# Performance work log

Hardware: AMD Instinct MI355X
Metric: run time of the kernel (lower is better)

## Reference

```python
import jax, jax.numpy as jnp
import numpy as np

N_USERS = 100000
N_ITEMS = 100000
NNZ = 3200000
D = 128

def _spmm(rows, cols, vals, dense, n_out):
    # COO SpMM: out[r] += vals * dense[c]
    gathered = dense[cols] * vals[:, None]  # [nnz, D]
    return jax.ops.segment_sum(gathered, rows, num_segments=n_out)

def setup_inputs() -> dict:
    key = jax.random.key(0)
    ks = jax.random.split(key, 7)
    return {
        "input": jax.random.normal(ks[0], (N_USERS + N_ITEMS, D), dtype=jnp.float32),
        "user_rows": jax.random.randint(ks[1], (NNZ,), 0, N_USERS, dtype=jnp.int32),
        "user_cols": jax.random.randint(ks[2], (NNZ,), 0, N_USERS, dtype=jnp.int32),
        "user_vals": jax.random.uniform(ks[3], (NNZ,), dtype=jnp.float32),
        "item_rows": jax.random.randint(ks[4], (NNZ,), 0, N_ITEMS, dtype=jnp.int32),
        "item_cols": jax.random.randint(ks[5], (NNZ,), 0, N_ITEMS, dtype=jnp.int32),
        "item_vals": jax.random.uniform(ks[6], (NNZ,), dtype=jnp.float32),
    }

def reference(input, user_rows, user_cols, user_vals, item_rows, item_cols, item_vals):
    users_emb = input[:N_USERS]          # [n_users, D]
    items_emb = input[N_USERS:]          # [n_items, D]
    h_u1 = _spmm(user_rows, user_cols, user_vals, users_emb, N_USERS)
    h_i1 = _spmm(item_rows, item_cols, item_vals, items_emb, N_ITEMS)
    return jnp.concatenate([h_u1, h_i1], axis=0)
```

## Files before the change

### kernel.cpp

```cpp
#include <hip/hip_runtime.h>

#define NU   100000
#define NI   100000
#define NNZE 3200000
#define D    128
#define CAPB 80

__device__ __forceinline__ unsigned bf15(float v) {
    return ((__float_as_uint(v) + 0x8000u) >> 16) & 0x7FFFu;
}
__device__ __forceinline__ unsigned bf16r(float x) {
    unsigned u = __float_as_uint(x);
    return (u + 0x7FFFu + ((u >> 16) & 1u)) >> 16;
}

__global__ void cvt_kernel(const float* __restrict__ in, unsigned short* __restrict__ outb) {
    const int total = (NU + NI) * D / 8;
    int gid = blockIdx.x * blockDim.x + threadIdx.x;
    const int stride = gridDim.x * blockDim.x;
    for (int i = gid; i < total; i += stride) {
        const float4 a = reinterpret_cast<const float4*>(in)[2 * i];
        const float4 b = reinterpret_cast<const float4*>(in)[2 * i + 1];
        uint4 w;
        w.x = bf16r(a.x) | (bf16r(a.y) << 16);
        w.y = bf16r(a.z) | (bf16r(a.w) << 16);
        w.z = bf16r(b.x) | (bf16r(b.y) << 16);
        w.w = bf16r(b.z) | (bf16r(b.w) << 16);
        reinterpret_cast<uint4*>(outb)[i] = w;
    }
}

__global__ void build_bins_kernel(const int* __restrict__ urows,
                                  const int* __restrict__ ucols,
                                  const float* __restrict__ uvals,
                                  const int* __restrict__ irows,
                                  const int* __restrict__ icols,
                                  const float* __restrict__ ivals,
                                  int* __restrict__ cnt_u, int* __restrict__ cnt_i,
                                  unsigned* __restrict__ bin_u, unsigned* __restrict__ bin_i,
                                  int cap) {
    int gid = blockIdx.x * blockDim.x + threadIdx.x;
    int stride = gridDim.x * blockDim.x;
    for (int e = gid; e < NNZE; e += stride) {
        int r = urows[e];
        int p = atomicAdd(&cnt_u[r], 1);
        if (p < cap) bin_u[(size_t)r * cap + p] = ((unsigned)ucols[e] << 15) | bf15(uvals[e]);
        r = irows[e];
        p = atomicAdd(&cnt_i[r], 1);
        if (p < cap) bin_i[(size_t)r * cap + p] = ((unsigned)icols[e] << 15) | bf15(ivals[e]);
    }
}

__global__ void pull_bf16_kernel(const unsigned short* __restrict__ tabb,
                                 const int* __restrict__ cnt_u, const int* __restrict__ cnt_i,
                                 const unsigned* __restrict__ bin_u,
                                 const unsigned* __restrict__ bin_i,
                                 float* __restrict__ out, int cap) {
    const int wid = (int)(((size_t)blockIdx.x * blockDim.x + threadIdx.x) >> 6);
    if (wid >= NU + NI) return;
    const int lane = threadIdx.x & 63;
    const int q    = lane >> 4;
    const int s16  = lane & 15;
    const int* cnt; const unsigned* bin; const unsigned short* src; float* dst; int row;
    if (wid < NU) {
        cnt = cnt_u; bin = bin_u; src = tabb; dst = out; row = wid;
    } else {
        cnt = cnt_i; bin = bin_i;
        src = tabb + (size_t)NU * D; dst = out + (size_t)NU * D; row = wid - NU;
    }
    int n = cnt[row];
    if (n > cap) n = cap;
    const unsigned* brow = bin + (size_t)row * cap;
    float acc[8];
#pragma unroll
    for (int k = 0; k < 8; ++k) acc[k] = 0.f;

    for (int base = 0; base < n; base += 64) {
        int m = n - base; if (m > 64) m = 64;
        unsigned ent = 0;
        if (lane < m) ent = brow[base + lane];
        const int   c = (int)(ent >> 15);
        const float v = __uint_as_float((ent & 0x7FFFu) << 16);

        int j = 0;
        for (; j + 8 <= m; j += 8) {
            const int   c0 = __shfl(c, j + q),     c1 = __shfl(c, j + 4 + q);
            const float v0 = __shfl(v, j + q),     v1 = __shfl(v, j + 4 + q);
            const uint4 x0 = reinterpret_cast<const uint4*>(src + (size_t)c0 * D)[s16];
            const uint4 x1 = reinterpret_cast<const uint4*>(src + (size_t)c1 * D)[s16];
#pragma unroll
            for (int t = 0; t < 4; ++t) {
                const unsigned u0 = (&x0.x)[t], u1 = (&x1.x)[t];
                acc[2*t]   += __uint_as_float(u0 << 16)         * v0;
                acc[2*t+1] += __uint_as_float(u0 & 0xFFFF0000u) * v0;
                acc[2*t]   += __uint_as_float(u1 << 16)         * v1;
                acc[2*t+1] += __uint_as_float(u1 & 0xFFFF0000u) * v1;
            }
        }
        for (; j + 4 <= m; j += 4) {
            const int   cc = __shfl(c, j + q);
            const float vv = __shfl(v, j + q);
            const uint4 x = reinterpret_cast<const uint4*>(src + (size_t)cc * D)[s16];
#pragma unroll
            for (int t = 0; t < 4; ++t) {
                const unsigned u = (&x.x)[t];
                acc[2*t]   += __uint_as_float(u << 16)         * vv;
                acc[2*t+1] += __uint_as_float(u & 0xFFFF0000u) * vv;
            }
        }
        if (j < m) {
            const int jj = j + q;
            const int   cc = __shfl(c, (jj < m) ? jj : j);
            const float vv = __shfl(v, (jj < m) ? jj : j);
            if (jj < m) {
                const uint4 x = reinterpret_cast<const uint4*>(src + (size_t)cc * D)[s16];
#pragma unroll
                for (int t = 0; t < 4; ++t) {
                    const unsigned u = (&x.x)[t];
                    acc[2*t]   += __uint_as_float(u << 16)         * vv;
                    acc[2*t+1] += __uint_as_float(u & 0xFFFF0000u) * vv;
                }
            }
        }
    }
#pragma unroll
    for (int k = 0; k < 8; ++k) {
        acc[k] += __shfl_xor(acc[k], 16);
        acc[k] += __shfl_xor(acc[k], 32);
    }
    if (q == 0) {
        float4 o0, o1;
        o0.x = acc[0]; o0.y = acc[1]; o0.z = acc[2]; o0.w = acc[3];
        o1.x = acc[4]; o1.y = acc[5]; o1.z = acc[6]; o1.w = acc[7];
        float4* op = reinterpret_cast<float4*>(dst + (size_t)row * D + 8 * s16);
        op[0] = o0; op[1] = o1;
    }
}

__global__ void hist_kernel(const int* __restrict__ urows,
                            const int* __restrict__ irows,
                            int* __restrict__ cnt_u, int* __restrict__ cnt_i) {
    int gid = blockIdx.x * blockDim.x + threadIdx.x;
    int stride = gridDim.x * blockDim.x;
    for (int e = gid; e < NNZE; e += stride) {
        atomicAdd(&cnt_u[urows[e]], 1);
        atomicAdd(&cnt_i[irows[e]], 1);
    }
}

__global__ void scan_kernel(int* __restrict__ cnt_u, int* __restrict__ off_u,
                            int* __restrict__ cnt_i, int* __restrict__ off_i) {
    int* cnt = (blockIdx.x == 0) ? cnt_u : cnt_i;
    int* off = (blockIdx.x == 0) ? off_u : off_i;
    const int n = (blockIdx.x == 0) ? NU : NI;
    __shared__ int lds[1024];
    int carry = 0;
    for (int base = 0; base < n; base += 1024) {
        const int i = base + (int)threadIdx.x;
        const int v = (i < n) ? cnt[i] : 0;
        lds[threadIdx.x] = v;
        __syncthreads();
        for (int ofs = 1; ofs < 1024; ofs <<= 1) {
            int t = (threadIdx.x >= (unsigned)ofs) ? lds[threadIdx.x - ofs] : 0;
            __syncthreads();
            lds[threadIdx.x] += t;
            __syncthreads();
        }
        const int incl = lds[threadIdx.x];
        const int excl = incl - v;
        if (i < n) {
            off[i] = carry + excl;
            cnt[i] = carry + excl;
        }
        carry += lds[1023];
        __syncthreads();
    }
    if (threadIdx.x == 0) off[n] = carry;
}

__global__ void scatter_kernel(const int* __restrict__ urows,
                               const int* __restrict__ irows,
                               int* __restrict__ cur_u, int* __restrict__ cur_i,
                               int* __restrict__ perm_u, int* __restrict__ perm_i) {
    int gid = blockIdx.x * blockDim.x + threadIdx.x;
    int stride = gridDim.x * blockDim.x;
    for (int e = gid; e < NNZE; e += stride) {
        int p = atomicAdd(&cur_u[urows[e]], 1);
        perm_u[p] = e;
        p = atomicAdd(&cur_i[irows[e]], 1);
        perm_i[p] = e;
    }
}

__global__ void pull_csr_kernel(const float* __restrict__ input,
                                const int* __restrict__ ucols, const float* __restrict__ uvals,
                                const int* __restrict__ icols, const float* __restrict__ ivals,
                                const int* __restrict__ off_u, const int* __restrict__ perm_u,
                                const int* __restrict__ off_i, const int* __restrict__ perm_i,
                                float* __restrict__ out) {
    const int wid = (int)(((size_t)blockIdx.x * blockDim.x + threadIdx.x) >> 6);
    if (wid >= NU + NI) return;
    const int lane = threadIdx.x & 63;
    const int* off; const int* perm; const int* cols; const float* vals;
    const float* src; float* dst; int row;
    if (wid < NU) {
        off = off_u; perm = perm_u; cols = ucols; vals = uvals;
        src = input; dst = out; row = wid;
    } else {
        off = off_i; perm = perm_i; cols = icols; vals = ivals;
        src = input + (size_t)NU * D; dst = out + (size_t)NU * D; row = wid - NU;
    }
    const int s = off[row];
    const int n = off[row + 1] - s;
    float accx = 0.f, accy = 0.f;
    for (int base = 0; base < n; base += 64) {
        int m = n - base; if (m > 64) m = 64;
        int c = 0; float v = 0.f;
        if (lane < m) {
            const int nz = perm[s + base + lane];
            c = cols[nz];
            v = vals[nz];
        }
        for (int j = 0; j < m; ++j) {
            const int   cc = __shfl(c, j);
            const float vv = __shfl(v, j);
            const float2 x = reinterpret_cast<const float2*>(src + (size_t)cc * D)[lane];
            accx += x.x * vv; accy += x.y * vv;
        }
    }
    float2 o; o.x = accx; o.y = accy;
    reinterpret_cast<float2*>(dst + (size_t)row * D)[lane] = o;
}

__global__ void spmm_scatter_kernel(const float* __restrict__ input,
                                    const int* __restrict__ urows,
                                    const int* __restrict__ ucols,
                                    const float* __restrict__ uvals,
                                    const int* __restrict__ irows,
                                    const int* __restrict__ icols,
                                    const float* __restrict__ ivals,
                                    float* __restrict__ out) {
    const long long total = 2LL * NNZE * 32;
    long long gid = (long long)blockIdx.x * blockDim.x + threadIdx.x;
    const long long stride = (long long)gridDim.x * blockDim.x;
    for (; gid < total; gid += stride) {
        const int e = (int)(gid >> 5);
        const int qq = (int)(gid & 31);
        int row, col; float val; const float* src; float* dst;
        if (e < NNZE) {
            row = urows[e]; col = ucols[e]; val = uvals[e];
            src = input; dst = out;
        } else {
            const int e2 = e - NNZE;
            row = irows[e2]; col = icols[e2]; val = ivals[e2];
            src = input + (long long)NU * D; dst = out + (long long)NU * D;
        }
        const float4 v = reinterpret_cast<const float4*>(src + (long long)col * D)[qq];
        float* o = dst + (long long)row * D + (qq << 2);
        atomicAdd(o + 0, v.x * val);
        atomicAdd(o + 1, v.y * val);
        atomicAdd(o + 2, v.z * val);
        atomicAdd(o + 3, v.w * val);
    }
}

extern "C" void kernel_launch(void* const* d_in, const int* in_sizes, int n_in,
                              void* d_out, int out_size, void* d_ws, size_t ws_size,
                              hipStream_t stream) {
    const float* input = (const float*)d_in[0];
    const int*   urows = (const int*)d_in[1];
    const int*   ucols = (const int*)d_in[2];
    const float* uvals = (const float*)d_in[3];
    const int*   irows = (const int*)d_in[4];
    const int*   icols = (const int*)d_in[5];
    const float* ivals = (const float*)d_in[6];
    float*       out   = (float*)d_out;

    const size_t need_t1 = (size_t)(NU + NI) * 4
                         + (size_t)(NU + NI) * D * 2
                         + (size_t)(NU + NI) * CAPB * 4;
    const size_t need_csr = ((size_t)NU + NI + (NU + 1) + (NI + 1) + 2 * (size_t)NNZE) * 4;

    if (ws_size >= need_t1) {
        int* cnt_u = (int*)d_ws;
        int* cnt_i = cnt_u + NU;
        unsigned short* tabb = (unsigned short*)(cnt_i + NI);
        unsigned* bin_u = (unsigned*)(tabb + (size_t)(NU + NI) * D);
        unsigned* bin_i = bin_u + (size_t)NU * CAPB;

        hipMemsetAsync(cnt_u, 0, (size_t)(NU + NI) * sizeof(int), stream);
        build_bins_kernel<<<4096, 256, 0, stream>>>(
            urows, ucols, uvals, irows, icols, ivals, cnt_u, cnt_i, bin_u, bin_i, CAPB);
        cvt_kernel<<<4096, 256, 0, stream>>>(input, tabb);
        const int blocks = (NU + NI + 3) / 4;
        pull_bf16_kernel<<<blocks, 256, 0, stream>>>(
            tabb, cnt_u, cnt_i, bin_u, bin_i, out, CAPB);
    } else if (ws_size >= need_csr) {
        int* cur_u  = (int*)d_ws;
        int* cur_i  = cur_u + NU;
        int* off_u  = cur_i + NI;
        int* off_i  = off_u + (NU + 1);
        int* perm_u = off_i + (NI + 1);
        int* perm_i = perm_u + NNZE;

        hipMemsetAsync(cur_u, 0, (size_t)(NU + NI) * sizeof(int), stream);
        hist_kernel<<<2048, 256, 0, stream>>>(urows, irows, cur_u, cur_i);
        scan_kernel<<<2, 1024, 0, stream>>>(cur_u, off_u, cur_i, off_i);
        scatter_kernel<<<2048, 256, 0, stream>>>(urows, irows, cur_u, cur_i, perm_u, perm_i);
        const int blocks = (NU + NI + 3) / 4;
        pull_csr_kernel<<<blocks, 256, 0, stream>>>(
            input, ucols, uvals, icols, ivals, off_u, perm_u, off_i, perm_i, out);
    } else {
        hipMemsetAsync(out, 0, (size_t)out_size * sizeof(float), stream);
        spmm_scatter_kernel<<<8192, 256, 0, stream>>>(
            input, urows, ucols, uvals, irows, icols, ivals, out);
    }
}
```

Baseline: 561.9 us.

## Partition bin-building atomics by row residue to localize them per XCD

The bin-build kernel now assigns each block a group g = blockIdx&7, and each block only handles edges whose row satisfies row&7==g. The counter array is re-indexed so each group's counters are contiguous. Since blocks are dispatched round-robin across the 8 XCDs, this aims to keep each counter's atomics and bin writes inside one XCD's L2, cutting cross-die coherence traffic. In exchange, every block reads all edge rows, so row-index reads rise eightfold, and col/val loads become divergent.

New measurement: 603.1 us. 1.07x slower.

```diff
diff --git a/kernel.cpp b/kernel.cpp
--- a/kernel.cpp
+++ b/kernel.cpp
@@ -5,6 +5,7 @@
 #define NNZE 3200000
 #define D    128
 #define CAPB 80
+#define GDIV 12500
 
 __device__ __forceinline__ unsigned bf15(float v) {
     return ((__float_as_uint(v) + 0x8000u) >> 16) & 0x7FFFu;
@@ -13,6 +14,7 @@
     unsigned u = __float_as_uint(x);
     return (u + 0x7FFFu + ((u >> 16) & 1u)) >> 16;
 }
+__device__ __forceinline__ int cidx(int r) { return (r & 7) * GDIV + (r >> 3); }
 
 __global__ void cvt_kernel(const float* __restrict__ in, unsigned short* __restrict__ outb) {
     const int total = (NU + NI) * D / 8;
@@ -30,24 +32,31 @@
     }
 }
 
-__global__ void build_bins_kernel(const int* __restrict__ urows,
-                                  const int* __restrict__ ucols,
-                                  const float* __restrict__ uvals,
-                                  const int* __restrict__ irows,
-                                  const int* __restrict__ icols,
-                                  const float* __restrict__ ivals,
-                                  int* __restrict__ cnt_u, int* __restrict__ cnt_i,
-                                  unsigned* __restrict__ bin_u, unsigned* __restrict__ bin_i,
-                                  int cap) {
-    int gid = blockIdx.x * blockDim.x + threadIdx.x;
-    int stride = gridDim.x * blockDim.x;
-    for (int e = gid; e < NNZE; e += stride) {
+__global__ void build_xcd_kernel(const int* __restrict__ urows,
+                                 const int* __restrict__ ucols,
+                                 const float* __restrict__ uvals,
+                                 const int* __restrict__ irows,
+                                 const int* __restrict__ icols,
+                                 const float* __restrict__ ivals,
+                                 int* __restrict__ cnt_u, int* __restrict__ cnt_i,
+                                 unsigned* __restrict__ bin_u, unsigned* __restrict__ bin_i) {
+    const int g  = blockIdx.x & 7;
+    const int nb = gridDim.x >> 3;
+    const int bi = blockIdx.x >> 3;
+    const int estride = nb * blockDim.x;
+    for (int e = bi * blockDim.x + threadIdx.x; e < NNZE; e += estride) {
         int r = urows[e];
-        int p = atomicAdd(&cnt_u[r], 1);
-        if (p < cap) bin_u[(size_t)r * cap + p] = ((unsigned)ucols[e] << 15) | bf15(uvals[e]);
+        if ((r & 7) == g) {
+            const unsigned ent = ((unsigned)ucols[e] << 15) | bf15(uvals[e]);
+            const int p = atomicAdd(&cnt_u[cidx(r)], 1);
+            if (p < CAPB) bin_u[(size_t)r * CAPB + p] = ent;
+        }
         r = irows[e];
-        p = atomicAdd(&cnt_i[r], 1);
-        if (p < cap) bin_i[(size_t)r * cap + p] = ((unsigned)icols[e] << 15) | bf15(ivals[e]);
+        if ((r & 7) == g) {
+            const unsigned ent = ((unsigned)icols[e] << 15) | bf15(ivals[e]);
+            const int p = atomicAdd(&cnt_i[cidx(r)], 1);
+            if (p < CAPB) bin_i[(size_t)r * CAPB + p] = ent;
+        }
     }
 }
 
@@ -55,7 +64,7 @@
                                  const int* __restrict__ cnt_u, const int* __restrict__ cnt_i,
                                  const unsigned* __restrict__ bin_u,
                                  const unsigned* __restrict__ bin_i,
-                                 float* __restrict__ out, int cap) {
+                                 float* __restrict__ out) {
     const int wid = (int)(((size_t)blockIdx.x * blockDim.x + threadIdx.x) >> 6);
     if (wid >= NU + NI) return;
     const int lane = threadIdx.x & 63;
@@ -68,9 +77,9 @@
         cnt = cnt_i; bin = bin_i;
         src = tabb + (size_t)NU * D; dst = out + (size_t)NU * D; row = wid - NU;
     }
-    int n = cnt[row];
-    if (n > cap) n = cap;
-    const unsigned* brow = bin + (size_t)row * cap;
+    int n = cnt[cidx(row)];
+    if (n > CAPB) n = CAPB;
+    const unsigned* brow = bin + (size_t)row * CAPB;
     float acc[8];
 #pragma unroll
     for (int k = 0; k < 8; ++k) acc[k] = 0.f;
@@ -289,12 +298,12 @@
         unsigned* bin_i = bin_u + (size_t)NU * CAPB;
 
         hipMemsetAsync(cnt_u, 0, (size_t)(NU + NI) * sizeof(int), stream);
-        build_bins_kernel<<<4096, 256, 0, stream>>>(
-            urows, ucols, uvals, irows, icols, ivals, cnt_u, cnt_i, bin_u, bin_i, CAPB);
+        build_xcd_kernel<<<4096, 256, 0, stream>>>(
+            urows, ucols, uvals, irows, icols, ivals, cnt_u, cnt_i, bin_u, bin_i);
         cvt_kernel<<<4096, 256, 0, stream>>>(input, tabb);
         const int blocks = (NU + NI + 3) / 4;
         pull_bf16_kernel<<<blocks, 256, 0, stream>>>(
-            tabb, cnt_u, cnt_i, bin_u, bin_i, out, CAPB);
+            tabb, cnt_u, cnt_i, bin_u, bin_i, out);
     } else if (ws_size >= need_csr) {
         int* cur_u  = (int*)d_ws;
         int* cur_i  = cur_u + NU;
```
